# Optimization experiments

Hardware: AMD Instinct MI355X
Metric: run time of the kernel (lower is better)

## Reference

```python
import jax, jax.numpy as jnp
import numpy as np

B, T, DH, DI, DO = 64, 1024, 512, 1, 1
DT = 1.0
PINH, PCON, G = 0.2, 0.8, 1.5
TAU_LO, TAU_HI = 4.0, 20.0
WOUT_SCL, X_NOISE_SCL = 100.0, 10.0
SEED = 1234


def setup_inputs() -> dict:
    key = jax.random.key(0)
    ks = jax.random.split(key, 7)
    rng = np.random.default_rng(SEED)
    # parameters (match torch init distributions)
    win = jax.random.normal(ks[0], (DH, DI), dtype=jnp.float32)
    m_np = np.eye(DH, dtype=np.float32)
    inh_idxs = rng.choice(DH, size=int(DH * PINH), replace=False)
    m_np[inh_idxs, inh_idxs] = -1.0
    m = jnp.asarray(m_np)
    wout = jax.random.normal(ks[1], (DO, DH), dtype=jnp.float32) / WOUT_SCL
    _w = jax.random.normal(ks[2], (DH, DH), dtype=jnp.float32) * (G / np.sqrt(DH * PCON))
    taus = jax.nn.sigmoid(jax.random.normal(ks[3], (DH, 1), dtype=jnp.float32)) * (TAU_HI - TAU_LO) + TAU_LO
    bias = jnp.zeros((DO, DO), dtype=jnp.float32)
    # forward inputs
    u = jax.random.normal(ks[4], (B, T, DI), dtype=jnp.float32)
    r0 = jax.random.normal(ks[5], (B, DH, 1), dtype=jnp.float32)
    # per-step noise, pre-sampled (torch samples inside the loop)
    noise = jax.random.normal(ks[6], (T, B, DH, 1), dtype=jnp.float32)
    return {"u": u, "r0": r0, "noise": noise, "win": win, "m": m,
            "wout": wout, "_w": _w, "taus": taus, "bias": bias}


def reference(u, r0, noise, win, m, wout, _w, taus, bias):
    # get_w with default nm_signal = identity: w = |_w @ m|
    w = jnp.abs(_w @ m)                      # (dh, dh)
    alpha = DT / taus                        # (dh, 1)
    u_seq = jnp.swapaxes(u, 0, 1)[:, :, None, :]  # (T, B, 1, di)

    def step(x_in, inp):
        u_t, n_t = inp                       # (B,1,di), (B,dh,1)
        r = jax.nn.sigmoid(x_in)             # (B, dh, 1)
        x_new = ((1.0 - alpha) * x_in
                 + alpha * jnp.einsum('hd,bde->bhe', w, r)
                 + jnp.einsum('hi,bie->bhe', win, u_t)
                 + n_t / X_NOISE_SCL)        # (B, dh, 1)
        out = jnp.einsum('oh,bhe->boe', wout, jax.nn.sigmoid(x_new)) + bias  # (B, do, 1)
        out = jnp.swapaxes(out, 1, 2)        # (B, 1, do)
        # faithful to torch: next step receives sigmoid(x_new) as its x
        return jax.nn.sigmoid(x_new), (out, x_new)

    _, (outs, xs) = jax.lax.scan(step, r0, (u_seq, noise))
    outputs = jnp.swapaxes(outs[:, :, 0, :], 0, 1)      # (B, T, do)
    xs_out = jnp.transpose(xs[..., 0], (1, 2, 0))       # (B, dh, T)
    return outputs, xs_out
```

## Files before the change

### kernel.cpp

```cpp
#include <hip/hip_runtime.h>

#define DHN 512
#define TN  1024
#define BN  64
#define CH  32
#define NLDSJ 12

static __device__ __forceinline__ float sigm(float x) {
  return 1.0f / (1.0f + __expf(-x));
}

#if defined(__has_builtin)
#if __has_builtin(__builtin_amdgcn_sdot4)
#define HAVE_SDOT4 1
#endif
#endif

static __device__ __forceinline__ int dot4(int a, int b, int c) {
#ifdef HAVE_SDOT4
  return __builtin_amdgcn_sdot4(a, b, c, false);
#else
  c += (int)(signed char)(a)       * (int)(signed char)(b);
  c += (int)(signed char)(a >> 8)  * (int)(signed char)(b >> 8);
  c += (int)(signed char)(a >> 16) * (int)(signed char)(b >> 16);
  c += (int)(signed char)(a >> 24) * (int)(signed char)(b >> 24);
  return c;
#endif
}

static __device__ __forceinline__ void lds_barrier() {
  __builtin_amdgcn_sched_barrier(0);
  asm volatile("s_waitcnt lgkmcnt(0)\n\ts_barrier" ::: "memory");
  __builtin_amdgcn_sched_barrier(0);
}

#define DPPADD(x, ctrl)                                                    \
  do {                                                                     \
    int _m = __builtin_amdgcn_update_dpp(0, __builtin_bit_cast(int, (x)),  \
                                         (ctrl), 0xF, 0xF, true);          \
    (x) += __builtin_bit_cast(float, _m);                                  \
  } while (0)

static __device__ __forceinline__ float wave_sum_lane63(float x) {
  DPPADD(x, 0x111);
  DPPADD(x, 0x112);
  DPPADD(x, 0x114);
  DPPADD(x, 0x118);
  DPPADD(x, 0x142);
  DPPADD(x, 0x143);
  return x;
}

__global__ __launch_bounds__(512) void k_rnn(
    const float* __restrict__ u, const float* __restrict__ r0,
    const float* __restrict__ noise, const float* __restrict__ win,
    const float* __restrict__ taus, const float* __restrict__ wmat,
    const float* __restrict__ wout, const float* __restrict__ bias,
    float* __restrict__ xs, float* __restrict__ outp) {
  __shared__ float u_lds[TN];
  __shared__ float nz_lds[CH * DHN];
  __shared__ __align__(16) signed char rbuf[2][DHN];
  __shared__ float part_lds[8][CH];

  const int h = threadIdx.x;
  const int lane = h & 63;
  const int wv = h >> 6;
  const int b = blockIdx.x;
  const float* wrow = wmat + h * DHN;

  float rmax = 1e-30f;
#pragma unroll 8
  for (int k = 0; k < 128; ++k) {
    float4 v = *(const float4*)(wrow + 4 * k);
    rmax = fmaxf(rmax, fabsf(v.x));
    rmax = fmaxf(rmax, fabsf(v.y));
    rmax = fmaxf(rmax, fabsf(v.z));
    rmax = fmaxf(rmax, fabsf(v.w));
  }
  const float qs = 127.0f / rmax;

  int w[128];
#pragma unroll
  for (int k = 0; k < 128; ++k) {
    float4 v = *(const float4*)(wrow + 4 * k);
    int q0 = __float2int_rn(fabsf(v.x) * qs);
    int q1 = __float2int_rn(fabsf(v.y) * qs);
    int q2 = __float2int_rn(fabsf(v.z) * qs);
    int q3 = __float2int_rn(fabsf(v.w) * qs);
    q0 = min(max(q0, 0), 127); q1 = min(max(q1, 0), 127);
    q2 = min(max(q2, 0), 127); q3 = min(max(q3, 0), 127);
    w[k] = q0 | (q1 << 8) | (q2 << 16) | (q3 << 24);
  }

  const float alpha  = 1.0f / taus[h];
  const float beta   = 1.0f - alpha;
  const float win_h  = win[h];
  const float wout_h = wout[h];
  const float bias0  = bias[0];
  const float dscale = rmax * alpha * (1.0f / 16129.0f);
  float s = r0[b * DHN + h];

  for (int i = h; i < TN; i += DHN) u_lds[i] = u[b * TN + i];
  rbuf[0][h] = (signed char)__float2int_rn(sigm(s) * 127.0f);

  const float* np = noise + (size_t)b * DHN + h;
  float* xrow = xs + ((size_t)b * DHN + h) * TN;

  float nreg[CH];
#pragma unroll
  for (int k = 0; k < CH; ++k) nreg[k] = np[(size_t)k * (BN * DHN)];

#pragma unroll 1
  for (int tc = 0; tc < TN; tc += CH) {
    __syncthreads();
    if (tc > 0 && h < CH) {
      float o = bias0;
#pragma unroll
      for (int wq = 0; wq < 8; ++wq) o += part_lds[wq][h];
      outp[b * TN + (tc - CH) + h] = o;
    }
#pragma unroll
    for (int k = 0; k < CH; ++k) nz_lds[k * DHN + h] = nreg[k];
    __syncthreads();
    if (tc + CH < TN) {
#pragma unroll
      for (int k = 0; k < CH; ++k)
        nreg[k] = np[(size_t)(tc + CH + k) * (BN * DHN)];
    }

#pragma unroll 1
    for (int t8 = 0; t8 < CH; t8 += 8) {
      float ua[8];
      *(float4*)&ua[0] = *(const float4*)&u_lds[tc + t8];
      *(float4*)&ua[4] = *(const float4*)&u_lds[tc + t8 + 4];
      float nzv[8];
#pragma unroll
      for (int e = 0; e < 8; ++e) nzv[e] = nz_lds[(t8 + e) * DHN + h];

      float xv[8];
#pragma unroll
      for (int e = 0; e < 8; ++e) {
        const signed char* rbp = &rbuf[e & 1][0];
        const int2 rv = *(const int2*)(rbp + 8 * lane);
        const int4* rb4 = (const int4*)rbp;
        int a0 = 0, a1 = 0, a2 = 0, a3 = 0;
#pragma unroll
        for (int j = 0; j < NLDSJ; ++j) {
          int4 rq = rb4[j];
          a0 = dot4(w[4 * j + 0], rq.x, a0);
          a1 = dot4(w[4 * j + 1], rq.y, a1);
          a2 = dot4(w[4 * j + 2], rq.z, a2);
          a3 = dot4(w[4 * j + 3], rq.w, a3);
        }
#pragma unroll
        for (int j = NLDSJ; j < 32; ++j) {
          const int rA0 = __builtin_amdgcn_readlane(rv.x, 2 * j);
          const int rB0 = __builtin_amdgcn_readlane(rv.y, 2 * j);
          const int rA1 = __builtin_amdgcn_readlane(rv.x, 2 * j + 1);
          const int rB1 = __builtin_amdgcn_readlane(rv.y, 2 * j + 1);
          a0 = dot4(w[4 * j + 0], rA0, a0);
          a1 = dot4(w[4 * j + 1], rB0, a1);
          a2 = dot4(w[4 * j + 2], rA1, a2);
          a3 = dot4(w[4 * j + 3], rB1, a3);
        }
        float x = beta * s + (float)((a0 + a1) + (a2 + a3)) * dscale
                + win_h * ua[e] + 0.1f * nzv[e];
        x = fminf(fmaxf(x, -40.0f), 40.0f);
        xv[e] = x;
        float sp = sigm(x);
        rbuf[(e & 1) ^ 1][h] =
            (signed char)__float2int_rn(sigm(sp) * 127.0f);
        s = sp;
        float po = wave_sum_lane63(wout_h * sp);
        if (lane == 63) part_lds[wv][t8 + e] = po;
        lds_barrier();
      }
      float4 p0 = {xv[0], xv[1], xv[2], xv[3]};
      float4 p1 = {xv[4], xv[5], xv[6], xv[7]};
      *(float4*)(xrow + tc + t8)     = p0;
      *(float4*)(xrow + tc + t8 + 4) = p1;
    }
  }
  __syncthreads();
  if (h < CH) {
    float o = bias0;
#pragma unroll
    for (int wq = 0; wq < 8; ++wq) o += part_lds[wq][h];
    outp[b * TN + (TN - CH) + h] = o;
  }
}

extern "C" void kernel_launch(void* const* d_in, const int* in_sizes, int n_in,
                              void* d_out, int out_size, void* d_ws, size_t ws_size,
                              hipStream_t stream) {
  const float* u     = (const float*)d_in[0];
  const float* r0    = (const float*)d_in[1];
  const float* noise = (const float*)d_in[2];
  const float* win   = (const float*)d_in[3];
  const float* wout  = (const float*)d_in[5];
  const float* w_    = (const float*)d_in[6];
  const float* taus  = (const float*)d_in[7];
  const float* bias  = (const float*)d_in[8];

  float* outp = (float*)d_out;
  float* xs   = outp + BN * TN;

  k_rnn<<<BN, DHN, 0, stream>>>(u, r0, noise, win, taus, w_, wout, bias,
                                xs, outp);
}
```

Measured before the change: 1.461 ms.

## Compute recurrent int8 matvec with MFMA 16x16x64 instead of per-thread sdot4

```diff
diff --git a/kernel.cpp b/kernel.cpp
--- a/kernel.cpp
+++ b/kernel.cpp
@@ -3,29 +3,12 @@
 #define DHN 512
 #define TN  1024
 #define BN  64
-#define CH  32
-#define NLDSJ 12
+#define CH  16
+
+typedef int int4v __attribute__((ext_vector_type(4)));
 
 static __device__ __forceinline__ float sigm(float x) {
   return 1.0f / (1.0f + __expf(-x));
-}
-
-#if defined(__has_builtin)
-#if __has_builtin(__builtin_amdgcn_sdot4)
-#define HAVE_SDOT4 1
-#endif
-#endif
-
-static __device__ __forceinline__ int dot4(int a, int b, int c) {
-#ifdef HAVE_SDOT4
-  return __builtin_amdgcn_sdot4(a, b, c, false);
-#else
-  c += (int)(signed char)(a)       * (int)(signed char)(b);
-  c += (int)(signed char)(a >> 8)  * (int)(signed char)(b >> 8);
-  c += (int)(signed char)(a >> 16) * (int)(signed char)(b >> 16);
-  c += (int)(signed char)(a >> 24) * (int)(signed char)(b >> 24);
-  return c;
-#endif
 }
 
 static __device__ __forceinline__ void lds_barrier() {
@@ -51,7 +34,7 @@
   return x;
 }
 
-__global__ __launch_bounds__(512) void k_rnn(
+__global__ __launch_bounds__(512, 2) void k_rnn(
     const float* __restrict__ u, const float* __restrict__ r0,
     const float* __restrict__ noise, const float* __restrict__ win,
     const float* __restrict__ taus, const float* __restrict__ wmat,
@@ -61,11 +44,15 @@
   __shared__ float nz_lds[CH * DHN];
   __shared__ __align__(16) signed char rbuf[2][DHN];
   __shared__ float part_lds[8][CH];
-
-  const int h = threadIdx.x;
+  __shared__ __align__(16) int dsum[DHN];
+  __shared__ float qs_lds[DHN];
+
+  const int h    = threadIdx.x;
   const int lane = h & 63;
-  const int wv = h >> 6;
-  const int b = blockIdx.x;
+  const int wv   = h >> 6;
+  const int lrow = lane & 15;
+  const int lkg  = lane >> 4;
+  const int b    = blockIdx.x;
   const float* wrow = wmat + h * DHN;
 
   float rmax = 1e-30f;
@@ -78,19 +65,7 @@
     rmax = fmaxf(rmax, fabsf(v.w));
   }
   const float qs = 127.0f / rmax;
-
-  int w[128];
-#pragma unroll
-  for (int k = 0; k < 128; ++k) {
-    float4 v = *(const float4*)(wrow + 4 * k);
-    int q0 = __float2int_rn(fabsf(v.x) * qs);
-    int q1 = __float2int_rn(fabsf(v.y) * qs);
-    int q2 = __float2int_rn(fabsf(v.z) * qs);
-    int q3 = __float2int_rn(fabsf(v.w) * qs);
-    q0 = min(max(q0, 0), 127); q1 = min(max(q1, 0), 127);
-    q2 = min(max(q2, 0), 127); q3 = min(max(q3, 0), 127);
-    w[k] = q0 | (q1 << 8) | (q2 << 16) | (q3 << 24);
-  }
+  qs_lds[h] = qs;
 
   const float alpha  = 1.0f / taus[h];
   const float beta   = 1.0f - alpha;
@@ -103,6 +78,31 @@
   for (int i = h; i < TN; i += DHN) u_lds[i] = u[b * TN + i];
   rbuf[0][h] = (signed char)__float2int_rn(sigm(s) * 127.0f);
 
+  __syncthreads();
+
+  int4v wfrag[4][8];
+#pragma unroll
+  for (int m = 0; m < 4; ++m) {
+    const int row = (wv * 4 + m) * 16 + lrow;
+    const float qsr = qs_lds[row];
+    const float* rp = wmat + (size_t)row * DHN + lkg * 16;
+#pragma unroll
+    for (int q = 0; q < 8; ++q) {
+      const float* cp = rp + q * 64;
+      int4v wd;
+#pragma unroll
+      for (int d = 0; d < 4; ++d) {
+        float4 v = *(const float4*)(cp + 4 * d);
+        int q0 = min(max(__float2int_rn(fabsf(v.x) * qsr), 0), 127);
+        int q1 = min(max(__float2int_rn(fabsf(v.y) * qsr), 0), 127);
+        int q2 = min(max(__float2int_rn(fabsf(v.z) * qsr), 0), 127);
+        int q3 = min(max(__float2int_rn(fabsf(v.w) * qsr), 0), 127);
+        wd[d] = q0 | (q1 << 8) | (q2 << 16) | (q3 << 24);
+      }
+      wfrag[m][q] = wd;
+    }
+  }
+
   const float* np = noise + (size_t)b * DHN + h;
   float* xrow = xs + ((size_t)b * DHN + h) * TN;
 
@@ -141,29 +141,29 @@
 #pragma unroll
       for (int e = 0; e < 8; ++e) {
         const signed char* rbp = &rbuf[e & 1][0];
-        const int2 rv = *(const int2*)(rbp + 8 * lane);
-        const int4* rb4 = (const int4*)rbp;
-        int a0 = 0, a1 = 0, a2 = 0, a3 = 0;
-#pragma unroll
-        for (int j = 0; j < NLDSJ; ++j) {
-          int4 rq = rb4[j];
-          a0 = dot4(w[4 * j + 0], rq.x, a0);
-          a1 = dot4(w[4 * j + 1], rq.y, a1);
-          a2 = dot4(w[4 * j + 2], rq.z, a2);
-          a3 = dot4(w[4 * j + 3], rq.w, a3);
+        int4v bq[8];
+#pragma unroll
+        for (int q = 0; q < 8; ++q)
+          bq[q] = *(const int4v*)(rbp + q * 64 + lkg * 16);
+
+        const int4v zz = {0, 0, 0, 0};
+        int4v acc[4];
+#pragma unroll
+        for (int m = 0; m < 4; ++m) acc[m] = zz;
+#pragma unroll
+        for (int q = 0; q < 8; ++q) {
+#pragma unroll
+          for (int m = 0; m < 4; ++m)
+            acc[m] = __builtin_amdgcn_mfma_i32_16x16x64_i8(
+                wfrag[m][q], bq[q], acc[m], 0, 0, 0);
         }
-#pragma unroll
-        for (int j = NLDSJ; j < 32; ++j) {
-          const int rA0 = __builtin_amdgcn_readlane(rv.x, 2 * j);
-          const int rB0 = __builtin_amdgcn_readlane(rv.y, 2 * j);
-          const int rA1 = __builtin_amdgcn_readlane(rv.x, 2 * j + 1);
-          const int rB1 = __builtin_amdgcn_readlane(rv.y, 2 * j + 1);
-          a0 = dot4(w[4 * j + 0], rA0, a0);
-          a1 = dot4(w[4 * j + 1], rB0, a1);
-          a2 = dot4(w[4 * j + 2], rA1, a2);
-          a3 = dot4(w[4 * j + 3], rB1, a3);
+        if (lrow == 0) {
+#pragma unroll
+          for (int m = 0; m < 4; ++m)
+            *(int4v*)&dsum[wv * 64 + m * 16 + lkg * 4] = acc[m];
         }
-        float x = beta * s + (float)((a0 + a1) + (a2 + a3)) * dscale
+        const int dot = dsum[h];
+        float x = beta * s + (float)dot * dscale
                 + win_h * ua[e] + 0.1f * nzv[e];
         x = fminf(fmaxf(x, -40.0f), 40.0f);
         xv[e] = x;
```

Result: faster. 1.234 ms (-15.5%).
